# Performance work log

Hardware: AMD Instinct MI355X
Metric: run time of the kernel (lower is better)

The kernel has to match this reference:

```python
import jax, jax.numpy as jnp
import numpy as np

NUM_EMBEDDINGS = 1024
EMBEDDING_DIM = 256
COMMITMENT_COST = 0.25


def setup_inputs() -> dict:
    key = jax.random.key(0)
    k1, k2 = jax.random.split(key)
    inputs = jax.random.normal(k1, (64, 1024, EMBEDDING_DIM), dtype=jnp.float32)
    # codebook initialized uniform(-1/K, 1/K) as in the torch module
    embedding = jax.random.uniform(
        k2, (NUM_EMBEDDINGS, EMBEDDING_DIM), dtype=jnp.float32,
        minval=-1.0 / NUM_EMBEDDINGS, maxval=1.0 / NUM_EMBEDDINGS)
    return {"inputs": inputs, "embedding": embedding}


def reference(inputs, embedding):
    # flatten to [N, D]
    D = embedding.shape[1]
    flat = inputs.reshape(-1, D)
    distances = (jnp.sum(flat * flat, axis=1, keepdims=True)
                 + jnp.sum(embedding * embedding, axis=1)
                 - 2.0 * jnp.matmul(flat, embedding.T))
    encoding_indices = jnp.argmin(distances, axis=1)  # [N]
    # one_hot @ embedding == gather; use gather (same math, no NxK one-hot)
    quantized = jnp.take(embedding, encoding_indices, axis=0).reshape(inputs.shape)
    # commitment loss: mse(stop_grad(quantized), inputs)
    e_latent_loss = jnp.mean(jnp.square(jax.lax.stop_gradient(quantized) - inputs))
    loss = COMMITMENT_COST * e_latent_loss
    # straight-through estimator
    quantized = inputs + jax.lax.stop_gradient(quantized - inputs)
    return quantized, loss, encoding_indices.reshape(inputs.shape[:-1])
```

## Files before the change

kernel.cpp:

```cpp
#include <hip/hip_runtime.h>
#include <cfloat>
#include <climits>

#define N_ROWS 65536
#define DIM 256
#define K_CODES 1024
#define N_ELEM 16777216
#define OUT_LOSS_OFF 16777216
#define OUT_IDX_OFF  16777217

#define ROWS_PB 128
#define CT 128
#define EPS_MARGIN 1.5e-4f
#define SHORTLIST_EPS 6e-4f
#define RB 8

#define WS_PARTIALS 0
#define WS_ESQ      8192
#define WS_IDX      12288
#define WS_FLAGCNT  274432
#define WS_FLAGLIST 274436
#define WS_EHI      540672
#define WS_ELO      1064960
#define WS_EHIT     1589248

typedef unsigned short u16;
typedef __attribute__((ext_vector_type(8))) short bf16x8;
typedef __attribute__((ext_vector_type(4))) float f32x4;
typedef union { bf16x8 v; unsigned u[4]; } frag_u;

__device__ __forceinline__ void glds16(const void* g, void* l) {
    __builtin_amdgcn_global_load_lds(
        (const __attribute__((address_space(1))) unsigned int*)g,
        (__attribute__((address_space(3))) unsigned int*)l,
        16, 0, 0);
}

__device__ __forceinline__ unsigned cvt_pk_bf16(float lo, float hi) {
    unsigned r;
    asm("v_cvt_pk_bf16_f32 %0, %1, %2" : "=v"(r) : "v"(lo), "v"(hi));
    return r;
}

__device__ __forceinline__ void split8(float4 a, float4 b, bf16x8& h8, bf16x8& l8) {
    frag_u H, L;
    float f0 = a.x, f1 = a.y, f2 = a.z, f3 = a.w;
    float f4 = b.x, f5 = b.y, f6 = b.z, f7 = b.w;
    const float* f[8] = {&f0,&f1,&f2,&f3,&f4,&f5,&f6,&f7};
    #pragma unroll
    for (int p = 0; p < 4; ++p) {
        float xl = *f[2*p], xh = *f[2*p+1];
        unsigned hw = cvt_pk_bf16(xl, xh);
        float hfl = __uint_as_float(hw << 16);
        float hfh = __uint_as_float(hw & 0xffff0000u);
        H.u[p] = hw;
        L.u[p] = cvt_pk_bf16(xl - hfl, xh - hfh);
    }
    h8 = H.v; l8 = L.v;
}

__device__ __forceinline__ void bsplit(float x, u16& h, u16& l) {
    unsigned u = __float_as_uint(x);
    unsigned hb = (u + 0x7fffu + ((u >> 16) & 1u)) >> 16;
    h = (u16)hb;
    float hf = __uint_as_float(hb << 16);
    float lf = x - hf;
    unsigned u2 = __float_as_uint(lf);
    l = (u16)((u2 + 0x7fffu + ((u2 >> 16) & 1u)) >> 16);
}

__device__ __forceinline__ float np_pairwise_sumsq(const float* __restrict__ a) {
    float half[2];
    #pragma unroll
    for (int h = 0; h < 2; ++h) {
        const float* p = a + h * 128;
        float r[8];
        #pragma unroll
        for (int j = 0; j < 8; ++j) r[j] = __fmul_rn(p[j], p[j]);
        for (int i = 8; i < 128; i += 8) {
            #pragma unroll
            for (int j = 0; j < 8; ++j)
                r[j] = __fadd_rn(r[j], __fmul_rn(p[i + j], p[i + j]));
        }
        half[h] = __fadd_rn(__fadd_rn(__fadd_rn(r[0], r[1]), __fadd_rn(r[2], r[3])),
                            __fadd_rn(__fadd_rn(r[4], r[5]), __fadd_rn(r[6], r[7])));
    }
    return __fadd_rn(half[0], half[1]);
}

__global__ void esplit_kernel(const float* __restrict__ e, u16* __restrict__ ehi,
                              u16* __restrict__ elo, u16* __restrict__ ehiT) {
    int i4 = blockIdx.x * 256 + threadIdx.x;
    float4 v = ((const float4*)e)[i4];
    ushort4 h, l;
    bsplit(v.x, h.x, l.x); bsplit(v.y, h.y, l.y);
    bsplit(v.z, h.z, l.z); bsplit(v.w, h.w, l.w);
    ((ushort4*)ehi)[i4] = h;
    ((ushort4*)elo)[i4] = l;
    int c = i4 >> 6;
    int f4 = i4 & 63;
    int qid = f4 >> 1;
    ((ushort4*)ehiT)[((size_t)qid * 1024 + c) * 2 + (f4 & 1)] = h;
}

__global__ void esq_kernel(const float* __restrict__ e, float* __restrict__ esq) {
    int c = blockIdx.x * 256 + threadIdx.x;
    if (c < K_CODES) esq[c] = np_pairwise_sumsq(e + c * DIM);
}

__launch_bounds__(512, 4)
__global__ void argmin_kernel(const float* __restrict__ x,
                              const u16* __restrict__ ehi, const u16* __restrict__ elo,
                              const float* __restrict__ esq, int* __restrict__ wsIdx,
                              int* __restrict__ flagCnt, int* __restrict__ flagList) {
    __shared__ __align__(16) unsigned char lds[65536];
    __shared__ float esq_s[CT];
    float* xSf  = (float*)lds;
    u16* ehiS = (u16*)(lds + 32768);
    u16* eloS = (u16*)(lds + 49152);

    const int t = threadIdx.x;
    const int w = t >> 6;
    const int l = t & 63;
    const int lane15 = l & 15;
    const int quad = l >> 4;
    const int rowBase = blockIdx.x * ROWS_PB;
    const int wr = w >> 1;
    const int wc = w & 1;

    float bv[8], sv[8]; int bi[8];
    #pragma unroll
    for (int i = 0; i < 8; ++i) { bv[i] = FLT_MAX; sv[i] = FLT_MAX; bi[i] = INT_MAX; }

    const int sub4 = l >> 4;
    const int jb16 = l & 15;
    const int sub8 = l >> 3;
    const int jb8 = l & 7;
    const int sb8 = jb8 ^ sub8;
    const u16* srcE = (w < 6) ? ehi : elo;
    u16* dstE = (w < 6) ? ehiS : eloS;
    const int halfE = w & 1;

    for (int ct = 0; ct < 8; ++ct) {
        const int ctBase = ct * CT;
        __syncthreads();
        if (t < CT) esq_s[t] = esq[ctBase + t];

        f32x4 acc[2][4];
        #pragma unroll
        for (int ti = 0; ti < 2; ++ti)
            #pragma unroll
            for (int tj = 0; tj < 4; ++tj) acc[ti][tj] = (f32x4){0.f, 0.f, 0.f, 0.f};

        for (int ch = 0; ch < 4; ++ch) {
            __syncthreads();
            if (w < 4) {
                #pragma unroll
                for (int i = 0; i < 8; ++i) {
                    int r = w * 32 + i * 4 + sub4;
                    int sbx = jb16 ^ (r & 15);
                    glds16(x + (size_t)(rowBase + r) * 256 + ch * 64 + sbx * 4,
                           (unsigned char*)lds + (w * 8 + i) * 1024);
                }
            } else {
                #pragma unroll
                for (int i = 0; i < 8; ++i) {
                    int r = halfE * 64 + i * 8 + sub8;
                    glds16(srcE + (size_t)(ctBase + r) * 256 + ch * 64 + sb8 * 8,
                           dstE + halfE * 4096 + i * 512);
                }
            }
            __syncthreads();

            #pragma unroll
            for (int kk = 0; kk < 2; ++kk) {
                bf16x8 ah[2], al4[2], bh[4], bl[4];
                const int blk = kk * 4 + quad;
                #pragma unroll
                for (int ti = 0; ti < 2; ++ti) {
                    int r = wr * 32 + ti * 16 + lane15;
                    int base = r * 64;
                    int s0 = ((2 * blk) ^ (r & 15)) * 4;
                    int s1 = ((2 * blk + 1) ^ (r & 15)) * 4;
                    float4 va = *(const float4*)(xSf + base + s0);
                    float4 vb = *(const float4*)(xSf + base + s1);
                    split8(va, vb, ah[ti], al4[ti]);
                }
                #pragma unroll
                for (int tj = 0; tj < 4; ++tj) {
                    int r = wc * 64 + tj * 16 + lane15;
                    int off = r * 64 + ((blk ^ (r & 7)) * 8);
                    bh[tj] = *(const bf16x8*)(ehiS + off);
                    bl[tj] = *(const bf16x8*)(eloS + off);
                }
                #pragma unroll
                for (int ti = 0; ti < 2; ++ti)
                    #pragma unroll
                    for (int tj = 0; tj < 4; ++tj) {
                        acc[ti][tj] = __builtin_amdgcn_mfma_f32_16x16x32_bf16(al4[ti], bh[tj], acc[ti][tj], 0, 0, 0);
                        acc[ti][tj] = __builtin_amdgcn_mfma_f32_16x16x32_bf16(ah[ti], bl[tj], acc[ti][tj], 0, 0, 0);
                        acc[ti][tj] = __builtin_amdgcn_mfma_f32_16x16x32_bf16(ah[ti], bh[tj], acc[ti][tj], 0, 0, 0);
                    }
            }
        }

        #pragma unroll
        for (int tj = 0; tj < 4; ++tj) {
            int cLoc = wc * 64 + tj * 16 + lane15;
            float cs = esq_s[cLoc];
            int c = ctBase + cLoc;
            #pragma unroll
            for (int ti = 0; ti < 2; ++ti)
                #pragma unroll
                for (int r4 = 0; r4 < 4; ++r4) {
                    int slot = ti * 4 + r4;
                    float s = fmaf(-2.0f, acc[ti][tj][r4], cs);
                    if (s < bv[slot]) {
                        sv[slot] = bv[slot]; bv[slot] = s; bi[slot] = c;
                    } else if (s < sv[slot]) {
                        sv[slot] = s;
                    }
                }
        }
    }

    __syncthreads();
    float* bvA = (float*)lds;
    float* svA = (float*)(lds + 16896);
    int*   biA = (int*)(lds + 33792);
    const int contrib = wc * 16 + lane15;
    #pragma unroll
    for (int slot = 0; slot < 8; ++slot) {
        int m = wr * 32 + (slot >> 2) * 16 + quad * 4 + (slot & 3);
        bvA[m * 33 + contrib] = bv[slot];
        svA[m * 33 + contrib] = sv[slot];
        biA[m * 33 + contrib] = bi[slot];
    }
    __syncthreads();

    if (t < ROWS_PB) {
        float bb = FLT_MAX, ss = FLT_MAX;
        int ii = INT_MAX;
        for (int k = 0; k < 32; ++k) {
            float v  = bvA[t * 33 + k];
            int   id = biA[t * 33 + k];
            float s2 = svA[t * 33 + k];
            if (v < bb || (v == bb && id < ii)) {
                ss = fminf(bb, s2);
                bb = v; ii = id;
            } else {
                ss = fminf(ss, v);
            }
        }
        int row = rowBase + t;
        wsIdx[row] = ii;
        if (ss - bb < EPS_MARGIN) {
            int p = atomicAdd(flagCnt, 1);
            flagList[p] = row;
        }
    }
}

__launch_bounds__(256)
__global__ void rescore_kernel(const float* __restrict__ x, const float* __restrict__ e,
                               const u16* __restrict__ ehiT, const float* __restrict__ esq,
                               int* __restrict__ wsIdx, const int* __restrict__ flagCnt,
                               const int* __restrict__ flagList) {
    __shared__ __align__(16) float xsh[RB][DIM];
    __shared__ float Ash[RB];
    __shared__ float minsh[RB][256];
    __shared__ float thrsh[RB];
    __shared__ int scnt[RB];
    __shared__ int slist[RB][32];
    __shared__ float sres[RB][32];
    const int t = threadIdx.x;
    const int cnt = *flagCnt;
    const int ngroups = (cnt + RB - 1) / RB;
    for (int g = blockIdx.x; g < ngroups; g += gridDim.x) {
        const int base = g * RB;
        const int nr = (cnt - base < RB) ? (cnt - base) : RB;
        __syncthreads();
        #pragma unroll
        for (int r = 0; r < RB; ++r)
            xsh[r][t] = (r < nr) ? x[(size_t)flagList[base + r] * DIM + t] : 0.0f;
        if (t < RB) scnt[t] = 0;
        __syncthreads();
        if (t < RB) Ash[t] = np_pairwise_sumsq(xsh[t]);

        float sA[4][RB];
        #pragma unroll
        for (int j = 0; j < 4; ++j)
            #pragma unroll
            for (int r = 0; r < RB; ++r) sA[j][r] = 0.0f;

        const uint4* eT4 = (const uint4*)ehiT;
        for (int q = 0; q < 32; ++q) {
            float4 xq[RB][2];
            #pragma unroll
            for (int r = 0; r < RB; ++r) {
                xq[r][0] = ((const float4*)xsh[r])[2 * q];
                xq[r][1] = ((const float4*)xsh[r])[2 * q + 1];
            }
            #pragma unroll
            for (int j = 0; j < 4; ++j) {
                uint4 uv = eT4[(size_t)q * 1024 + j * 256 + t];
                float e0 = __uint_as_float(uv.x << 16);
                float e1 = __uint_as_float(uv.x & 0xffff0000u);
                float e2 = __uint_as_float(uv.y << 16);
                float e3 = __uint_as_float(uv.y & 0xffff0000u);
                float e4v = __uint_as_float(uv.z << 16);
                float e5 = __uint_as_float(uv.z & 0xffff0000u);
                float e6 = __uint_as_float(uv.w << 16);
                float e7 = __uint_as_float(uv.w & 0xffff0000u);
                #pragma unroll
                for (int r = 0; r < RB; ++r) {
                    float d0 = sA[j][r];
                    d0 = fmaf(e0, xq[r][0].x, d0);
                    d0 = fmaf(e1, xq[r][0].y, d0);
                    d0 = fmaf(e2, xq[r][0].z, d0);
                    d0 = fmaf(e3, xq[r][0].w, d0);
                    d0 = fmaf(e4v, xq[r][1].x, d0);
                    d0 = fmaf(e5, xq[r][1].y, d0);
                    d0 = fmaf(e6, xq[r][1].z, d0);
                    d0 = fmaf(e7, xq[r][1].w, d0);
                    sA[j][r] = d0;
                }
            }
        }
        #pragma unroll
        for (int j = 0; j < 4; ++j) {
            float cs = esq[j * 256 + t];
            #pragma unroll
            for (int r = 0; r < RB; ++r)
                sA[j][r] = fmaf(-2.0f, sA[j][r], cs);
        }
        #pragma unroll
        for (int r = 0; r < RB; ++r)
            minsh[r][t] = fminf(fminf(sA[0][r], sA[1][r]), fminf(sA[2][r], sA[3][r]));
        __syncthreads();
        for (int off = 128; off > 0; off >>= 1) {
            if (t < off) {
                #pragma unroll
                for (int r = 0; r < RB; ++r)
                    minsh[r][t] = fminf(minsh[r][t], minsh[r][t + off]);
            }
            __syncthreads();
        }
        if (t < RB) thrsh[t] = minsh[t][0] + SHORTLIST_EPS;
        __syncthreads();
        #pragma unroll
        for (int j = 0; j < 4; ++j)
            #pragma unroll
            for (int r = 0; r < RB; ++r)
                if (r < nr && sA[j][r] <= thrsh[r]) {
                    int p = atomicAdd(&scnt[r], 1);
                    if (p < 32) slist[r][p] = j * 256 + t;
                }
        __syncthreads();
        {
            int r = t >> 5, k = t & 31;
            int ns = scnt[r] < 32 ? scnt[r] : 32;
            if (r < nr && k < ns) {
                int c = slist[r][k];
                const float4* ec4 = (const float4*)(e + (size_t)c * DIM);
                const float4* xc4 = (const float4*)xsh[r];
                double dot = 0.0;
                #pragma unroll 8
                for (int d4 = 0; d4 < 64; ++d4) {
                    float4 ev = ec4[d4];
                    float4 xv = xc4[d4];
                    dot += (double)ev.x * (double)xv.x + (double)ev.y * (double)xv.y
                         + (double)ev.z * (double)xv.z + (double)ev.w * (double)xv.w;
                }
                float M = (float)dot;
                sres[r][k] = __fsub_rn(__fadd_rn(Ash[r], esq[c]), __fmul_rn(2.0f, M));
            }
        }
        __syncthreads();
        if (t < nr) {
            int ns = scnt[t] < 32 ? scnt[t] : 32;
            float bb = FLT_MAX; int ii = INT_MAX;
            for (int k = 0; k < ns; ++k) {
                float s = sres[t][k]; int c = slist[t][k];
                if (s < bb || (s == bb && c < ii)) { bb = s; ii = c; }
            }
            wsIdx[flagList[base + t]] = ii;
        }
    }
}

__global__ void gather_kernel(const float* __restrict__ x, const float* __restrict__ e,
                              const int* __restrict__ wsIdx, float* __restrict__ out,
                              double* __restrict__ partials) {
    const float4* x4 = (const float4*)x;
    const float4* e4 = (const float4*)e;
    float4* q4 = (float4*)out;
    float* outIdx = out + OUT_IDX_OFF;
    const int tid = blockIdx.x * 256 + threadIdx.x;
    double sse = 0.0;
    #pragma unroll 4
    for (int i = 0; i < 16; ++i) {
        int u = tid + i * 262144;
        int row = u >> 6;
        int c4 = u & 63;
        int idx = wsIdx[row];
        float4 q = e4[idx * 64 + c4];
        float4 xv = x4[u];
        q4[u] = q;
        double dx = (double)q.x - (double)xv.x;
        double dy = (double)q.y - (double)xv.y;
        double dz = (double)q.z - (double)xv.z;
        double dw = (double)q.w - (double)xv.w;
        sse += dx * dx + dy * dy + dz * dz + dw * dw;
    }
    if (tid < N_ROWS) outIdx[tid] = (float)wsIdx[tid];
    #pragma unroll
    for (int m = 1; m < 64; m <<= 1) sse += __shfl_xor(sse, m);
    __shared__ double wsum[4];
    if ((threadIdx.x & 63) == 0) wsum[threadIdx.x >> 6] = sse;
    __syncthreads();
    if (threadIdx.x == 0)
        partials[blockIdx.x] = wsum[0] + wsum[1] + wsum[2] + wsum[3];
}

__global__ void loss_kernel(const double* __restrict__ partials, float* __restrict__ out) {
    __shared__ double sh[256];
    const int t = threadIdx.x;
    double s = partials[t] + partials[t + 256] + partials[t + 512] + partials[t + 768];
    sh[t] = s;
    __syncthreads();
    for (int off = 128; off > 0; off >>= 1) {
        if (t < off) sh[t] += sh[t + off];
        __syncthreads();
    }
    if (t == 0) out[OUT_LOSS_OFF] = (float)(0.25 * sh[0] / (double)N_ELEM);
}

extern "C" void kernel_launch(void* const* d_in, const int* in_sizes, int n_in,
                              void* d_out, int out_size, void* d_ws, size_t ws_size,
                              hipStream_t stream) {
    (void)in_sizes; (void)n_in; (void)out_size; (void)ws_size;
    const float* x = (const float*)d_in[0];
    const float* e = (const float*)d_in[1];
    float* out = (float*)d_out;
    char* ws = (char*)d_ws;
    double* partials = (double*)(ws + WS_PARTIALS);
    float* esq = (float*)(ws + WS_ESQ);
    int* wsIdx = (int*)(ws + WS_IDX);
    int* flagCnt = (int*)(ws + WS_FLAGCNT);
    int* flagList = (int*)(ws + WS_FLAGLIST);
    u16* ehi = (u16*)(ws + WS_EHI);
    u16* elo = (u16*)(ws + WS_ELO);
    u16* ehiT = (u16*)(ws + WS_EHIT);

    hipMemsetAsync(flagCnt, 0, sizeof(int), stream);
    esplit_kernel<<<256, 256, 0, stream>>>(e, ehi, elo, ehiT);
    esq_kernel<<<4, 256, 0, stream>>>(e, esq);
    argmin_kernel<<<N_ROWS / ROWS_PB, 512, 0, stream>>>(x, ehi, elo, esq,
                                                        wsIdx, flagCnt, flagList);
    rescore_kernel<<<512, 256, 0, stream>>>(x, e, ehiT, esq, wsIdx, flagCnt, flagList);
    gather_kernel<<<1024, 256, 0, stream>>>(x, e, wsIdx, out, partials);
    loss_kernel<<<1, 256, 0, stream>>>(partials, out);
}
```

Measured before the change: 313.7 us.

## Pre-split x tile into bf16 hi/lo in LDS and fuse codebook prep kernels

The argmin kernel now loads each x chunk through registers with all 512 threads, splits it into bf16 hi/lo once, and stores both halves to LDS. Previously four waves copied raw fp32 into LDS and every consuming wave re-split it for each MFMA tile. This removes the repeated split work and halves the LDS bytes read per fragment. The cost is that x goes through a synchronous register path instead of direct global-to-LDS loads. Separately, the esplit, esq and memset launches are merged into one eprep kernel to cut launch overhead.

```diff
diff --git a/kernel.cpp b/kernel.cpp
--- a/kernel.cpp
+++ b/kernel.cpp
@@ -88,24 +88,28 @@
     return __fadd_rn(half[0], half[1]);
 }
 
-__global__ void esplit_kernel(const float* __restrict__ e, u16* __restrict__ ehi,
-                              u16* __restrict__ elo, u16* __restrict__ ehiT) {
-    int i4 = blockIdx.x * 256 + threadIdx.x;
-    float4 v = ((const float4*)e)[i4];
-    ushort4 h, l;
-    bsplit(v.x, h.x, l.x); bsplit(v.y, h.y, l.y);
-    bsplit(v.z, h.z, l.z); bsplit(v.w, h.w, l.w);
-    ((ushort4*)ehi)[i4] = h;
-    ((ushort4*)elo)[i4] = l;
-    int c = i4 >> 6;
-    int f4 = i4 & 63;
-    int qid = f4 >> 1;
-    ((ushort4*)ehiT)[((size_t)qid * 1024 + c) * 2 + (f4 & 1)] = h;
-}
-
-__global__ void esq_kernel(const float* __restrict__ e, float* __restrict__ esq) {
-    int c = blockIdx.x * 256 + threadIdx.x;
-    if (c < K_CODES) esq[c] = np_pairwise_sumsq(e + c * DIM);
+__launch_bounds__(256)
+__global__ void eprep_kernel(const float* __restrict__ e, u16* __restrict__ ehi,
+                             u16* __restrict__ elo, u16* __restrict__ ehiT,
+                             float* __restrict__ esqOut, int* __restrict__ flagCnt) {
+    const int b = blockIdx.x;
+    if (b < 256) {
+        int i4 = b * 256 + threadIdx.x;
+        float4 v = ((const float4*)e)[i4];
+        ushort4 h, l;
+        bsplit(v.x, h.x, l.x); bsplit(v.y, h.y, l.y);
+        bsplit(v.z, h.z, l.z); bsplit(v.w, h.w, l.w);
+        ((ushort4*)ehi)[i4] = h;
+        ((ushort4*)elo)[i4] = l;
+        int c = i4 >> 6;
+        int f4 = i4 & 63;
+        int qid = f4 >> 1;
+        ((ushort4*)ehiT)[((size_t)qid * 1024 + c) * 2 + (f4 & 1)] = h;
+    } else {
+        if (b == 256 && threadIdx.x == 0) *flagCnt = 0;
+        int c = (b - 256) * 256 + threadIdx.x;
+        if (c < K_CODES) esqOut[c] = np_pairwise_sumsq(e + c * DIM);
+    }
 }
 
 __launch_bounds__(512, 4)
@@ -115,7 +119,8 @@
                               int* __restrict__ flagCnt, int* __restrict__ flagList) {
     __shared__ __align__(16) unsigned char lds[65536];
     __shared__ float esq_s[CT];
-    float* xSf  = (float*)lds;
+    u16* xhiS = (u16*)lds;
+    u16* xloS = (u16*)(lds + 16384);
     u16* ehiS = (u16*)(lds + 32768);
     u16* eloS = (u16*)(lds + 49152);
 
@@ -132,8 +137,6 @@
     #pragma unroll
     for (int i = 0; i < 8; ++i) { bv[i] = FLT_MAX; sv[i] = FLT_MAX; bi[i] = INT_MAX; }
 
-    const int sub4 = l >> 4;
-    const int jb16 = l & 15;
     const int sub8 = l >> 3;
     const int jb8 = l & 7;
     const int sb8 = jb8 ^ sub8;
@@ -141,6 +144,11 @@
     u16* dstE = (w < 6) ? ehiS : eloS;
     const int halfE = w & 1;
 
+    const int g0 = t;
+    const int g1 = 512 + t;
+    const int r0 = g0 >> 3, jb0 = g0 & 7, sb0 = jb0 ^ (r0 & 7);
+    const int r1 = g1 >> 3, jb1 = g1 & 7, sb1 = jb1 ^ (r1 & 7);
+
     for (int ct = 0; ct < 8; ++ct) {
         const int ctBase = ct * CT;
         __syncthreads();
@@ -154,15 +162,11 @@
 
         for (int ch = 0; ch < 4; ++ch) {
             __syncthreads();
-            if (w < 4) {
-                #pragma unroll
-                for (int i = 0; i < 8; ++i) {
-                    int r = w * 32 + i * 4 + sub4;
-                    int sbx = jb16 ^ (r & 15);
-                    glds16(x + (size_t)(rowBase + r) * 256 + ch * 64 + sbx * 4,
-                           (unsigned char*)lds + (w * 8 + i) * 1024);
-                }
-            } else {
+            const float4* gp0 = (const float4*)(x + (size_t)(rowBase + r0) * 256 + ch * 64 + sb0 * 8);
+            const float4* gp1 = (const float4*)(x + (size_t)(rowBase + r1) * 256 + ch * 64 + sb1 * 8);
+            float4 va0 = gp0[0], vb0 = gp0[1];
+            float4 va1 = gp1[0], vb1 = gp1[1];
+            if (w >= 4) {
                 #pragma unroll
                 for (int i = 0; i < 8; ++i) {
                     int r = halfE * 64 + i * 8 + sub8;
@@ -170,6 +174,15 @@
                            dstE + halfE * 4096 + i * 512);
                 }
             }
+            {
+                bf16x8 h8, l8;
+                split8(va0, vb0, h8, l8);
+                *(bf16x8*)(xhiS + r0 * 64 + jb0 * 8) = h8;
+                *(bf16x8*)(xloS + r0 * 64 + jb0 * 8) = l8;
+                split8(va1, vb1, h8, l8);
+                *(bf16x8*)(xhiS + r1 * 64 + jb1 * 8) = h8;
+                *(bf16x8*)(xloS + r1 * 64 + jb1 * 8) = l8;
+            }
             __syncthreads();
 
             #pragma unroll
@@ -179,12 +192,9 @@
                 #pragma unroll
                 for (int ti = 0; ti < 2; ++ti) {
                     int r = wr * 32 + ti * 16 + lane15;
-                    int base = r * 64;
-                    int s0 = ((2 * blk) ^ (r & 15)) * 4;
-                    int s1 = ((2 * blk + 1) ^ (r & 15)) * 4;
-                    float4 va = *(const float4*)(xSf + base + s0);
-                    float4 vb = *(const float4*)(xSf + base + s1);
-                    split8(va, vb, ah[ti], al4[ti]);
+                    int off = r * 64 + ((blk ^ (r & 7)) * 8);
+                    ah[ti]  = *(const bf16x8*)(xhiS + off);
+                    al4[ti] = *(const bf16x8*)(xloS + off);
                 }
                 #pragma unroll
                 for (int tj = 0; tj < 4; ++tj) {
@@ -453,9 +463,7 @@
     u16* elo = (u16*)(ws + WS_ELO);
     u16* ehiT = (u16*)(ws + WS_EHIT);
 
-    hipMemsetAsync(flagCnt, 0, sizeof(int), stream);
-    esplit_kernel<<<256, 256, 0, stream>>>(e, ehi, elo, ehiT);
-    esq_kernel<<<4, 256, 0, stream>>>(e, esq);
+    eprep_kernel<<<260, 256, 0, stream>>>(e, ehi, elo, ehiT, esq, flagCnt);
     argmin_kernel<<<N_ROWS / ROWS_PB, 512, 0, stream>>>(x, ehi, elo, esq,
                                                         wsIdx, flagCnt, flagList);
     rescore_kernel<<<512, 256, 0, stream>>>(x, e, ehiT, esq, wsIdx, flagCnt, flagList);
```

Result: faster. 299.8 us (-4.4%).
